# Performance work log

Hardware: AMD Instinct MI355X
Metric: run time of the kernel (lower is better)

## Reference

```python
import jax, jax.numpy as jnp
import numpy as np

# near_sym_b (13,19)-tap biorthogonal level-1 DTCWT filters (Kingsbury)
H0O = np.array([-0.0017578125, 0.0, 0.022265625, -0.046875, -0.0482421875,
                0.296875, 0.5554687500, 0.296875, -0.0482421875, -0.046875,
                0.022265625, 0.0, -0.0017578125], dtype=np.float32)
H1O = np.array([-7.0626e-05, 0.0, 1.34189e-03, -1.88341e-03, -7.15660e-03,
                2.38560e-02, 5.56431e-02, -5.16881e-02, -2.99758e-01,
                5.59431e-01, -2.99758e-01, -5.16881e-02, 5.56431e-02,
                2.38560e-02, -7.15660e-03, -1.88341e-03, 1.34189e-03,
                0.0, -7.0626e-05], dtype=np.float32)

def _alt(h):
    c = (len(h) - 1) // 2
    return (h * ((-1.0) ** (np.arange(len(h)) - c))).astype(np.float32)

G0O = _alt(H1O)  # synthesis lowpass  (PR complement of H1O)
G1O = _alt(H0O)  # synthesis highpass (PR complement of H0O)

DIM, HS, WS, BATCH, NB, BS = 64, 56, 56, 32, 4, 16


def _filt(x, h, axis):
    # depthwise 1D correlation with symmetric padding; x: (B,C,H,W), axis in {2,3}
    L = len(h); p = L // 2
    pad = [(0, 0)] * 4; pad[axis] = (p, p)
    xp = jnp.pad(x, pad, mode='symmetric')
    k = jnp.asarray(h, x.dtype).reshape((1, 1, L, 1) if axis == 2 else (1, 1, 1, L))
    B, C = x.shape[:2]
    y = jax.lax.conv_general_dilated(
        xp.reshape((B * C, 1) + xp.shape[2:]), k, (1, 1), 'VALID',
        dimension_numbers=('NCHW', 'OIHW', 'NCHW'))
    return y.reshape((B, C) + y.shape[2:])


def _q2c(y):
    y = y * np.float32(1.0 / np.sqrt(2.0))
    a = y[..., 0::2, 0::2]; b = y[..., 0::2, 1::2]
    c = y[..., 1::2, 0::2]; d = y[..., 1::2, 1::2]
    return (a - d, b + c), (a + d, b - c)


def _c2q(w1r, w1i, w2r, w2i):
    sc = np.float32(1.0 / np.sqrt(2.0))
    B, C, Hh, Wh = w1r.shape
    top = jnp.stack([(w1r + w2r) * sc, (w1i + w2i) * sc], axis=-1).reshape(B, C, Hh, 2 * Wh)
    bot = jnp.stack([(w1i - w2i) * sc, (w2r - w1r) * sc], axis=-1).reshape(B, C, Hh, 2 * Wh)
    return jnp.stack([top, bot], axis=3).reshape(B, C, 2 * Hh, 2 * Wh)


def dtcwt_fwd_j1(x):
    lo = _filt(x, H0O, 3); hi = _filt(x, H1O, 3)
    ll = _filt(lo, H0O, 2)
    (d15r, d15i), (d165r, d165i) = _q2c(_filt(lo, H1O, 2))   # LH -> 15/165 deg
    (d75r, d75i), (d105r, d105i) = _q2c(_filt(hi, H0O, 2))   # HL -> 75/105 deg
    (d45r, d45i), (d135r, d135i) = _q2c(_filt(hi, H1O, 2))   # HH -> 45/135 deg
    real = jnp.stack([d15r, d45r, d75r, d105r, d135r, d165r], axis=2)
    imag = jnp.stack([d15i, d45i, d75i, d105i, d135i, d165i], axis=2)
    return ll, jnp.stack([real, imag], axis=-1)  # (B,C,H,W), (B,C,6,H/2,W/2,2)


def dtcwt_inv_j1(ll, yh):
    r = yh[..., 0]; im = yh[..., 1]
    lh = _c2q(r[:, :, 0], im[:, :, 0], r[:, :, 5], im[:, :, 5])
    hl = _c2q(r[:, :, 2], im[:, :, 2], r[:, :, 3], im[:, :, 3])
    hh = _c2q(r[:, :, 1], im[:, :, 1], r[:, :, 4], im[:, :, 4])
    lo = _filt(ll, G0O, 2) + _filt(lh, G1O, 2)
    hi = _filt(hl, G0O, 2) + _filt(hh, G1O, 2)
    return _filt(lo, G0O, 3) + _filt(hi, G1O, 3)


def setup_inputs():
    key = jax.random.key(0)
    ks = jax.random.split(key, 6)
    return {
        'x': jax.random.normal(ks[0], (BATCH, HS * WS, DIM), jnp.float32),
        'w_ll': jax.random.normal(ks[1], (DIM, HS, WS), jnp.float32) * 0.02,
        'w1': jax.random.normal(ks[2], (2, NB, BS, BS), jnp.float32) * 0.02,
        'w2': jax.random.normal(ks[3], (2, NB, BS, BS), jnp.float32) * 0.02,
        'b1': jax.random.normal(ks[4], (2, NB, BS), jnp.float32) * 0.02,
        'b2': jax.random.normal(ks[5], (2, NB, BS), jnp.float32) * 0.02,
        'H': HS, 'W': WS,
    }


def reference(x, w_ll, w1, w2, b1, b2, H, W):
    Bt, N, C = x.shape
    xi = jnp.transpose(x.reshape(Bt, H, W, C), (0, 3, 1, 2)).astype(jnp.float32)
    xl, xh = dtcwt_fwd_j1(xi)
    xl = xl * w_ll                                  # (B,C,H,W) * (C,H,W)
    Hh, Wh = H // 2, W // 2
    # (B,C,6,Hh,Wh,2) -> (2,B,6,Hh,Wh,C) -> split C into (NB,BS) blocks
    xh = jnp.transpose(xh, (5, 0, 2, 3, 4, 1)).reshape(2, Bt, 6, Hh, Wh, NB, BS)
    xr, xim = xh[0], xh[1]
    mul = lambda t, w: jnp.einsum('...bd,bdk->...bk', t, w)
    r1 = jax.nn.relu(mul(xr, w1[0]) - mul(xim, w1[1]) + b1[0])
    i1 = jax.nn.relu(mul(xr, w1[1]) + mul(xim, w1[0]) + b1[1])
    r2 = mul(r1, w2[0]) - mul(i1, w2[1]) + b2[0]
    i2 = mul(r1, w2[1]) + mul(i1, w2[0]) + b2[1]
    xh2 = jnp.stack([r2, i2], axis=-1).reshape(Bt, 6, Hh, Wh, C, 2)
    xh2 = jnp.transpose(xh2, (0, 4, 1, 2, 3, 5))    # (B,C,6,Hh,Wh,2)
    y = dtcwt_inv_j1(xl, xh2)
    return jnp.transpose(y, (0, 2, 3, 1)).reshape(Bt, N, C)
```

## Files before the change

### kernel.cpp

```cpp
#include <hip/hip_runtime.h>

#define BT 32
#define CH 64
#define HS 56
#define WS 56
#define HH 28
#define WH 28

namespace {
constexpr float ISQ2 = 0.70710678118654752440f;
constexpr float F_H0[13] = {-0.0017578125f, 0.0f, 0.022265625f, -0.046875f,
    -0.0482421875f, 0.296875f, 0.55546875f, 0.296875f, -0.0482421875f,
    -0.046875f, 0.022265625f, 0.0f, -0.0017578125f};
constexpr float F_H1[19] = {-7.0626e-05f, 0.0f, 0.00134189f, -0.00188341f,
    -0.0071566f, 0.023856f, 0.0556431f, -0.0516881f, -0.299758f, 0.559431f,
    -0.299758f, -0.0516881f, 0.0556431f, 0.023856f, -0.0071566f,
    -0.00188341f, 0.00134189f, 0.0f, -7.0626e-05f};
constexpr float F_G0[19] = {7.0626e-05f, 0.0f, -0.00134189f, -0.00188341f,
    0.0071566f, 0.023856f, -0.0556431f, -0.0516881f, 0.299758f, 0.559431f,
    0.299758f, -0.0516881f, -0.0556431f, 0.023856f, 0.0071566f,
    -0.00188341f, -0.00134189f, 0.0f, 7.0626e-05f};
constexpr float F_G1[13] = {-0.0017578125f, 0.0f, 0.022265625f, 0.046875f,
    -0.0482421875f, -0.296875f, 0.55546875f, -0.296875f, -0.0482421875f,
    0.046875f, 0.022265625f, 0.0f, -0.0017578125f};
}

__device__ __forceinline__ int symi(int k) {
    k = (k < 0) ? (-1 - k) : k;
    k = (k >= HS) ? (2 * HS - 1 - k) : k;
    return k;
}

__device__ __forceinline__ unsigned short f2bf(float f) {
    unsigned u = __float_as_uint(f);
    u += 0x7fffu + ((u >> 16) & 1u);
    return (unsigned short)(u >> 16);
}
__device__ __forceinline__ float bf2f(unsigned short h) {
    return __uint_as_float(((unsigned)h) << 16);
}
__device__ __forceinline__ float2 bfp2(unsigned u) {
    float2 r;
    r.x = __uint_as_float((u & 0xffffu) << 16);
    r.y = __uint_as_float(u & 0xffff0000u);
    return r;
}
__device__ __forceinline__ unsigned packbf(float a, float b) {
    return (unsigned)f2bf(a) | ((unsigned)f2bf(b) << 16);
}

typedef __attribute__((ext_vector_type(8))) short short8;
typedef __attribute__((ext_vector_type(4))) float f32x4;

#define PPOS 784

__global__ __launch_bounds__(256) void k_fwd_rows(const float* __restrict__ x,
                                                  unsigned short* __restrict__ lo,
                                                  unsigned short* __restrict__ hi,
                                                  const float* __restrict__ wll,
                                                  float* __restrict__ wllT) {
    int b = blockIdx.x / HS, h = blockIdx.x % HS;
    int strip = threadIdx.x >> 5;
    int c0 = (threadIdx.x & 31) * 2;
    int base = (b * HS + h) * WS * CH + c0;
    const float* row = x + base;
    unsigned short* lop = lo + base;
    unsigned short* hip = hi + base;
    int w0s = strip * 7;
    float Wa[19], Wb[19];
#pragma unroll
    for (int t = 0; t < 19; ++t) {
        float2 v = *(const float2*)(row + symi(w0s - 9 + t) * CH);
        Wa[t] = v.x; Wb[t] = v.y;
    }
    float2 nW[7];
#pragma unroll
    for (int u = 0; u < 7; ++u) nW[u] = *(const float2*)(row + symi(w0s + u + 10) * CH);
#pragma unroll
    for (int u = 0; u < 7; ++u) {
        int w = w0s + u;
        float aLo = 0.f, aHi = 0.f, bLo = 0.f, bHi = 0.f;
#pragma unroll
        for (int t = 0; t < 13; ++t) { aLo += F_H0[t] * Wa[3 + t]; bLo += F_H0[t] * Wb[3 + t]; }
#pragma unroll
        for (int t = 0; t < 19; ++t) { aHi += F_H1[t] * Wa[t]; bHi += F_H1[t] * Wb[t]; }
        *(unsigned*)(lop + w * CH) = packbf(aLo, bLo);
        *(unsigned*)(hip + w * CH) = packbf(aHi, bHi);
#pragma unroll
        for (int t = 0; t < 18; ++t) { Wa[t] = Wa[t + 1]; Wb[t] = Wb[t + 1]; }
        Wa[18] = nW[u].x; Wb[18] = nW[u].y;
    }
    if (blockIdx.x < 49) {
        __shared__ float tile[64][65];
        int pos0 = blockIdx.x * 64;
        int lp = threadIdx.x & 63, g = threadIdx.x >> 6;
#pragma unroll
        for (int r = 0; r < 16; ++r) {
            int cc = r * 4 + g;
            tile[cc][lp] = wll[cc * (HS * WS) + pos0 + lp];
        }
        __syncthreads();
#pragma unroll
        for (int r = 0; r < 16; ++r) {
            int pl = r * 4 + g;
            wllT[(pos0 + pl) * CH + lp] = tile[lp][pl];
        }
    }
}

__global__ __launch_bounds__(256) void k_cols(
    const unsigned short* __restrict__ lo_in,
    const unsigned short* __restrict__ hi_in, const float* __restrict__ wllT,
    unsigned short* __restrict__ xl, unsigned short* __restrict__ sbT) {
    __shared__ unsigned short qTb[2][4][14][64];
    int hf = blockIdx.y;
    int zmode = blockIdx.z;
    int b = blockIdx.x / WH, wp = blockIdx.x % WH;
    int w0 = 2 * wp, tid = threadIdx.x;
    int q = tid >> 6, c = tid & 63;
    int rp = q >> 1, jc = q & 1;
    const unsigned short* srcp = zmode ? hi_in : lo_in;
    const unsigned short* colbase = srcp + (b * HS) * WS * CH + (w0 + jc) * CH + c;
    {
        int hstart = 2 * (hf * 14) + rp;
        float W[19];
#pragma unroll
        for (int t = 0; t < 19; ++t) W[t] = bf2f(colbase[symi(hstart - 9 + t) * (WS * CH)]);
        for (int rnd = 0; rnd < 2; ++rnd) {
            float nW0[7], nW1[7], nwll[7];
            int ii0 = rnd * 7;
#pragma unroll
            for (int u = 0; u < 7; ++u) {
                int h = hstart + 2 * (ii0 + u);
                nW0[u] = bf2f(colbase[symi(h + 10) * (WS * CH)]);
                nW1[u] = bf2f(colbase[symi(h + 11) * (WS * CH)]);
            }
            if (zmode == 0) {
#pragma unroll
                for (int u = 0; u < 7; ++u)
                    nwll[u] = wllT[((hstart + 2 * (ii0 + u)) * WS + (w0 + jc)) * CH + c];
            }
#pragma unroll
            for (int u = 0; u < 7; ++u) {
                int ii = ii0 + u;
                int h = hstart + 2 * ii;
                float v0 = 0.f, v1 = 0.f;
#pragma unroll
                for (int t = 0; t < 13; ++t) v0 += F_H0[t] * W[3 + t];
#pragma unroll
                for (int t = 0; t < 19; ++t) v1 += F_H1[t] * W[t];
                if (zmode == 0) {
                    xl[((b * HS + h) * WS + (w0 + jc)) * CH + c] = f2bf(v0 * nwll[u]);
                    qTb[0][q][ii][c] = f2bf(v1);
                } else {
                    qTb[0][q][ii][c] = f2bf(v0);
                    qTb[1][q][ii][c] = f2bf(v1);
                }
#pragma unroll
                for (int t = 0; t < 17; ++t) W[t] = W[t + 2];
                W[17] = nW0[u];
                W[18] = nW1[u];
            }
        }
    }
    __syncthreads();
    {
        int qq = tid >> 5;
        int role = qq & 3, half = qq >> 2;
        int c0 = (tid & 31) * 2;
        int rowA = role & 1, rowB = 3 - (role & 1);
        float sgn = (role == 1 || role == 2) ? 1.f : -1.f;
        int posb = wp * 28 + hf * 14;
        if (zmode == 0) {
            int p = (role < 2) ? role : role + 8;
            unsigned short* dst = sbT + ((p * BT + b) * PPOS + posb) * CH + c0;
#pragma unroll
            for (int g = 0; g < 7; ++g) {
                int ii = half * 7 + g;
                float2 av = bfp2(*(const unsigned*)&qTb[0][rowA][ii][c0]);
                float2 bv = bfp2(*(const unsigned*)&qTb[0][rowB][ii][c0]);
                float v0 = (av.x + sgn * bv.x) * ISQ2;
                float v1 = (av.y + sgn * bv.y) * ISQ2;
                *(unsigned*)(dst + ii * CH) = packbf(v0, v1);
            }
        } else {
#pragma unroll
            for (int src = 0; src < 2; ++src) {
                int p = (src == 0) ? (4 + role) : ((role < 2) ? (2 + role) : (6 + role));
                unsigned short* dst = sbT + ((p * BT + b) * PPOS + posb) * CH + c0;
#pragma unroll
                for (int g = 0; g < 7; ++g) {
                    int ii = half * 7 + g;
                    float2 av = bfp2(*(const unsigned*)&qTb[src][rowA][ii][c0]);
                    float2 bv = bfp2(*(const unsigned*)&qTb[src][rowB][ii][c0]);
                    float v0 = (av.x + sgn * bv.x) * ISQ2;
                    float v1 = (av.y + sgn * bv.y) * ISQ2;
                    *(unsigned*)(dst + ii * CH) = packbf(v0, v1);
                }
            }
        }
    }
}

__global__ __launch_bounds__(256) void k_mix(
    const unsigned short* __restrict__ sbT, const float* __restrict__ w1,
    const float* __restrict__ w2, const float* __restrict__ b1,
    const float* __restrict__ b2, unsigned short* __restrict__ P0,
    unsigned short* __restrict__ P1, unsigned short* __restrict__ P2) {
    __shared__ unsigned short l1a[4][16][36];
    __shared__ unsigned short l1b[4][16][36];
    int blk = blockIdx.x;
    int pr = blk / (BT * 49);
    int rem = blk % (BT * 49);
    int b = rem / 49;
    int tile = rem % 49;
    int sa = (pr == 0) ? 0 : (pr == 1) ? 2 : 1;
    int sb = (pr == 0) ? 5 : (pr == 1) ? 3 : 4;
    unsigned short* Pd = (pr == 0) ? P0 : (pr == 1) ? P1 : P2;
    int tid = threadIdx.x;
    int lane = tid & 63;
    int wv = tid >> 6;
    int nb = __builtin_amdgcn_readfirstlane(wv);
    int quad = lane >> 4;
    int n = lane & 15;

    int rix = quad >> 1, dlo = (quad & 1) * 8;
    int pos0 = tile * 16;
    const unsigned short* pAa =
        sbT + (((sa * 2 + rix) * BT + b) * PPOS + pos0 + n) * CH + nb * 16 + dlo;
    const unsigned short* pAb =
        sbT + (((sb * 2 + rix) * BT + b) * PPOS + pos0 + n) * CH + nb * 16 + dlo;
    short8 A1a = *(const short8*)pAa;
    short8 A1b = *(const short8*)pAb;

    short8 B1r, B1i, B2r, B2i;
#pragma unroll
    for (int j = 0; j < 8; ++j) {
        int kk = quad * 8 + j;
        int riw = kk >> 4, dd = kk & 15;
        float v1r = w1[nb * 256 + dd * 16 + n];
        float v1i = w1[1024 + nb * 256 + dd * 16 + n];
        float v2r = w2[nb * 256 + dd * 16 + n];
        float v2i = w2[1024 + nb * 256 + dd * 16 + n];
        B1r[j] = (short)f2bf(riw ? -v1i : v1r);
        B1i[j] = (short)f2bf(riw ? v1r : v1i);
        B2r[j] = (short)f2bf(riw ? -v2i : v2r);
        B2i[j] = (short)f2bf(riw ? v2r : v2i);
    }
    float bias1r = b1[nb * 16 + n], bias1i = b1[64 + nb * 16 + n];
    float bias2r = b2[nb * 16 + n], bias2i = b2[64 + nb * 16 + n];

    f32x4 a1r = {bias1r, bias1r, bias1r, bias1r};
    f32x4 a1i = {bias1i, bias1i, bias1i, bias1i};
    f32x4 b1r_ = a1r, b1i_ = a1i;
    a1r = __builtin_amdgcn_mfma_f32_16x16x32_bf16(A1a, B1r, a1r, 0, 0, 0);
    a1i = __builtin_amdgcn_mfma_f32_16x16x32_bf16(A1a, B1i, a1i, 0, 0, 0);
    b1r_ = __builtin_amdgcn_mfma_f32_16x16x32_bf16(A1b, B1r, b1r_, 0, 0, 0);
    b1i_ = __builtin_amdgcn_mfma_f32_16x16x32_bf16(A1b, B1i, b1i_, 0, 0, 0);
#pragma unroll
    for (int r = 0; r < 4; ++r) {
        int pos = quad * 4 + r;
        l1a[wv][pos][n] = f2bf(fmaxf(a1r[r], 0.f));
        l1a[wv][pos][16 + n] = f2bf(fmaxf(a1i[r], 0.f));
        l1b[wv][pos][n] = f2bf(fmaxf(b1r_[r], 0.f));
        l1b[wv][pos][16 + n] = f2bf(fmaxf(b1i_[r], 0.f));
    }
    union { short8 s8; uint2 u2[2]; } a2a, a2b;
    const unsigned short* rowpa = &l1a[wv][n][0];
    const unsigned short* rowpb = &l1b[wv][n][0];
    a2a.u2[0] = *(const uint2*)(rowpa + quad * 8);
    a2a.u2[1] = *(const uint2*)(rowpa + quad * 8 + 4);
    a2b.u2[0] = *(const uint2*)(rowpb + quad * 8);
    a2b.u2[1] = *(const uint2*)(rowpb + quad * 8 + 4);
    f32x4 aAr = {bias2r, bias2r, bias2r, bias2r};
    f32x4 aAi = {bias2i, bias2i, bias2i, bias2i};
    f32x4 aBr = aAr, aBi = aAi;
    aAr = __builtin_amdgcn_mfma_f32_16x16x32_bf16(a2a.s8, B2r, aAr, 0, 0, 0);
    aAi = __builtin_amdgcn_mfma_f32_16x16x32_bf16(a2a.s8, B2i, aAi, 0, 0, 0);
    aBr = __builtin_amdgcn_mfma_f32_16x16x32_bf16(a2b.s8, B2r, aBr, 0, 0, 0);
    aBi = __builtin_amdgcn_mfma_f32_16x16x32_bf16(a2b.s8, B2i, aBi, 0, 0, 0);
#pragma unroll
    for (int r = 0; r < 4; ++r) {
        int pos_g = pos0 + quad * 4 + r;
        int wp = pos_g / 28, ii = pos_g - wp * 28;
        int o = ((b * HS + 2 * ii) * WS + 2 * wp) * CH + nb * 16 + n;
        Pd[o] = f2bf((aAr[r] + aBr[r]) * ISQ2);
        Pd[o + CH] = f2bf((aAi[r] + aBi[r]) * ISQ2);
        Pd[o + WS * CH] = f2bf((aAi[r] - aBi[r]) * ISQ2);
        Pd[o + WS * CH + CH] = f2bf((aBr[r] - aAr[r]) * ISQ2);
    }
}

template <int MODE>
__device__ __forceinline__ void inv_cols_body(
    const unsigned short* __restrict__ xl, const unsigned short* __restrict__ P0,
    const unsigned short* __restrict__ P1, const unsigned short* __restrict__ P2,
    unsigned short* __restrict__ lo2, unsigned short* __restrict__ hi2) {
    int hf = blockIdx.y;
    int b = blockIdx.x / 7, wg = blockIdx.x % 7;
    int wl = threadIdx.x >> 5, l = threadIdx.x & 31;
    int c0 = l * 2;
    int w = wg * 8 + wl;
    int base = (b * HS) * WS * CH + w * CH + c0;
    const int st = WS * CH;
    const unsigned short* Ap = (MODE == 0) ? xl : P1;
    const unsigned short* Bp = (MODE == 0) ? P0 : P2;
    unsigned short* outp = (MODE == 0) ? lo2 : hi2;
    auto ldA = [&](int r) -> float2 {
        return bfp2(*(const unsigned*)(Ap + base + r * st));
    };
    auto ldB = [&](int r) -> float2 {
        return bfp2(*(const unsigned*)(Bp + base + r * st));
    };
    int h0 = hf * 14;
    float Aa[19], Ab[19], Ba[13], Bb[13];
#pragma unroll
    for (int t = 0; t < 19; ++t) { float2 v = ldA(symi(h0 - 9 + t)); Aa[t] = v.x; Ab[t] = v.y; }
#pragma unroll
    for (int t = 0; t < 13; ++t) { float2 v = ldB(symi(h0 - 6 + t)); Ba[t] = v.x; Bb[t] = v.y; }
    float2 pa0[4], pb0[4], pa1[4], pb1[4];
#define LDG(bA, bB, OFF, CNT)                                                   \
    {                                                                           \
        _Pragma("unroll") for (int u = 0; u < (CNT); ++u)                       \
            bA[u] = ldA(symi(h0 + (OFF) + u + 10));                             \
        _Pragma("unroll") for (int u = 0; u < (CNT); ++u)                       \
            bB[u] = ldB(symi(h0 + (OFF) + u + 7));                              \
    }
#define CPG(bA, bB, OFF, CNT)                                                   \
    {                                                                           \
        _Pragma("unroll") for (int u = 0; u < (CNT); ++u) {                     \
            int h = h0 + (OFF) + u;                                             \
            float acca = 0.f, accb = 0.f;                                       \
            _Pragma("unroll") for (int t = 0; t < 19; ++t) {                    \
                acca += F_G0[t] * Aa[t]; accb += F_G0[t] * Ab[t];               \
            }                                                                   \
            _Pragma("unroll") for (int t = 0; t < 13; ++t) {                    \
                acca += F_G1[t] * Ba[t]; accb += F_G1[t] * Bb[t];               \
            }                                                                   \
            *(unsigned*)(outp + base + h * st) = packbf(acca, accb);            \
            _Pragma("unroll") for (int t = 0; t < 18; ++t) {                    \
                Aa[t] = Aa[t + 1]; Ab[t] = Ab[t + 1];                           \
            }                                                                   \
            _Pragma("unroll") for (int t = 0; t < 12; ++t) {                    \
                Ba[t] = Ba[t + 1]; Bb[t] = Bb[t + 1];                           \
            }                                                                   \
            Aa[18] = bA[u].x; Ab[18] = bA[u].y;                                 \
            Ba[12] = bB[u].x; Bb[12] = bB[u].y;                                 \
        }                                                                       \
    }
    LDG(pa0, pb0, 0, 4) LDG(pa1, pb1, 4, 4)
    CPG(pa0, pb0, 0, 4) LDG(pa0, pb0, 8, 4)
    CPG(pa1, pb1, 4, 4) LDG(pa1, pb1, 12, 2)
    CPG(pa0, pb0, 8, 4)
    CPG(pa1, pb1, 12, 2)
#undef LDG
#undef CPG
}

__global__ __launch_bounds__(256) void k_inv_cols(
    const unsigned short* __restrict__ xl, const unsigned short* __restrict__ P0,
    const unsigned short* __restrict__ P1, const unsigned short* __restrict__ P2,
    unsigned short* __restrict__ lo2, unsigned short* __restrict__ hi2) {
    if (blockIdx.z == 0)
        inv_cols_body<0>(xl, P0, P1, P2, lo2, hi2);
    else
        inv_cols_body<1>(xl, P0, P1, P2, lo2, hi2);
}

__global__ __launch_bounds__(256) void k_inv_rows(
    const unsigned short* __restrict__ lo2,
    const unsigned short* __restrict__ hi2, float* __restrict__ out) {
    int b = blockIdx.x / HS, h = blockIdx.x % HS;
    int strip = threadIdx.x >> 5;
    int c0 = (threadIdx.x & 31) * 2;
    int base = (b * HS + h) * WS * CH + c0;
    const unsigned short* rlo = lo2 + base;
    const unsigned short* rhi = hi2 + base;
    float* op = out + base;
    int w0s = strip * 7;
    float Aa[19], Ab[19], Ba[13], Bb[13];
#pragma unroll
    for (int t = 0; t < 19; ++t) {
        float2 v = bfp2(*(const unsigned*)(rlo + symi(w0s - 9 + t) * CH));
        Aa[t] = v.x; Ab[t] = v.y;
    }
#pragma unroll
    for (int t = 0; t < 13; ++t) {
        float2 v = bfp2(*(const unsigned*)(rhi + symi(w0s - 6 + t) * CH));
        Ba[t] = v.x; Bb[t] = v.y;
    }
    float2 nA[7], nB[7];
#pragma unroll
    for (int u = 0; u < 7; ++u) nA[u] = bfp2(*(const unsigned*)(rlo + symi(w0s + u + 10) * CH));
#pragma unroll
    for (int u = 0; u < 7; ++u) nB[u] = bfp2(*(const unsigned*)(rhi + symi(w0s + u + 7) * CH));
#pragma unroll
    for (int u = 0; u < 7; ++u) {
        int w = w0s + u;
        float acca = 0.f, accb = 0.f;
#pragma unroll
        for (int t = 0; t < 19; ++t) { acca += F_G0[t] * Aa[t]; accb += F_G0[t] * Ab[t]; }
#pragma unroll
        for (int t = 0; t < 13; ++t) { acca += F_G1[t] * Ba[t]; accb += F_G1[t] * Bb[t]; }
        float2 ov; ov.x = acca; ov.y = accb;
        *(float2*)(op + w * CH) = ov;
#pragma unroll
        for (int t = 0; t < 18; ++t) { Aa[t] = Aa[t + 1]; Ab[t] = Ab[t + 1]; }
#pragma unroll
        for (int t = 0; t < 12; ++t) { Ba[t] = Ba[t + 1]; Bb[t] = Bb[t + 1]; }
        Aa[18] = nA[u].x; Ab[18] = nA[u].y;
        Ba[12] = nB[u].x; Bb[12] = nB[u].y;
    }
}

extern "C" void kernel_launch(void* const* d_in, const int* in_sizes, int n_in,
                              void* d_out, int out_size, void* d_ws, size_t ws_size,
                              hipStream_t stream) {
    const float* x = (const float*)d_in[0];
    const float* w_ll = (const float*)d_in[1];
    const float* w1 = (const float*)d_in[2];
    const float* w2 = (const float*)d_in[3];
    const float* b1 = (const float*)d_in[4];
    const float* b2 = (const float*)d_in[5];
    float* out = (float*)d_out;

    const size_t A = (size_t)BT * HS * WS * CH;
    const size_t SBf = (size_t)12 * 64 * BT * PPOS / 2;
    float* wsf = (float*)d_ws;
    unsigned short* xl = (unsigned short*)wsf;
    unsigned short* sbT = (unsigned short*)(wsf + A);
    unsigned short* lo2 = (unsigned short*)(wsf + A);
    unsigned short* hi2 = (unsigned short*)(wsf + A + SBf);
    unsigned short* lo_in = (unsigned short*)(wsf + A + SBf + A);
    unsigned short* hi_in = lo_in + A;
    unsigned short* P0 = hi_in + A;
    unsigned short* P1 = P0 + A;
    unsigned short* P2 = P1 + A;

    float* wllT = out;

    k_fwd_rows<<<BT * HS, 256, 0, stream>>>(x, lo_in, hi_in, w_ll, wllT);
    k_cols<<<dim3(BT * WH, 2, 2), 256, 0, stream>>>(lo_in, hi_in, wllT, xl, sbT);
    k_mix<<<3 * BT * 49, 256, 0, stream>>>(sbT, w1, w2, b1, b2, P0, P1, P2);
    k_inv_cols<<<dim3(BT * 7, 4, 2), 256, 0, stream>>>(xl, P0, P1, P2, lo2, hi2);
    k_inv_rows<<<BT * HS, 256, 0, stream>>>(lo2, hi2, out);
}
```

Baseline: 169.2 us.

## Fuse column filtering and complex channel-mix MLP into one kernel

Merges k_cols and k_mix so the subband quadrature outputs stay in LDS (pA) and feed the MFMA-based complex mixing directly, instead of being written to the sbT global buffer and read back. This removes one kernel launch and a full round trip of subband data through global memory. In exchange, each block handles only 14 positions per 16-row MFMA tile, so some MFMA work is wasted on padding rows. The l1a/l1b staging now aliases the qTb buffer after a barrier, and the mix work is split unevenly between the zmode blocks.

```diff
diff --git a/kernel.cpp b/kernel.cpp
--- a/kernel.cpp
+++ b/kernel.cpp
@@ -108,11 +108,19 @@
     }
 }
 
-__global__ __launch_bounds__(256) void k_cols(
+__global__ __launch_bounds__(256) void k_cols_mix(
     const unsigned short* __restrict__ lo_in,
     const unsigned short* __restrict__ hi_in, const float* __restrict__ wllT,
-    unsigned short* __restrict__ xl, unsigned short* __restrict__ sbT) {
-    __shared__ unsigned short qTb[2][4][14][64];
+    const float* __restrict__ w1, const float* __restrict__ w2,
+    const float* __restrict__ b1, const float* __restrict__ b2,
+    unsigned short* __restrict__ xl, unsigned short* __restrict__ P0,
+    unsigned short* __restrict__ P1, unsigned short* __restrict__ P2) {
+    __shared__ __align__(16) unsigned short qTb[2][4][14][64];
+    __shared__ __align__(16) unsigned short pA[8][14][72];
+    unsigned short (*l1a)[16][36] =
+        reinterpret_cast<unsigned short(*)[16][36]>(&qTb[0][0][0][0]);
+    unsigned short (*l1b)[16][36] = l1a + 4;
+
     int hf = blockIdx.y;
     int zmode = blockIdx.z;
     int b = blockIdx.x / WH, wp = blockIdx.x % WH;
@@ -170,10 +178,7 @@
         int c0 = (tid & 31) * 2;
         int rowA = role & 1, rowB = 3 - (role & 1);
         float sgn = (role == 1 || role == 2) ? 1.f : -1.f;
-        int posb = wp * 28 + hf * 14;
         if (zmode == 0) {
-            int p = (role < 2) ? role : role + 8;
-            unsigned short* dst = sbT + ((p * BT + b) * PPOS + posb) * CH + c0;
 #pragma unroll
             for (int g = 0; g < 7; ++g) {
                 int ii = half * 7 + g;
@@ -181,13 +186,12 @@
                 float2 bv = bfp2(*(const unsigned*)&qTb[0][rowB][ii][c0]);
                 float v0 = (av.x + sgn * bv.x) * ISQ2;
                 float v1 = (av.y + sgn * bv.y) * ISQ2;
-                *(unsigned*)(dst + ii * CH) = packbf(v0, v1);
+                *(unsigned*)&pA[role][ii][c0] = packbf(v0, v1);
             }
         } else {
 #pragma unroll
             for (int src = 0; src < 2; ++src) {
-                int p = (src == 0) ? (4 + role) : ((role < 2) ? (2 + role) : (6 + role));
-                unsigned short* dst = sbT + ((p * BT + b) * PPOS + posb) * CH + c0;
+                int pl = (src == 0) ? (2 + role) : ((role < 2) ? role : (4 + role));
 #pragma unroll
                 for (int g = 0; g < 7; ++g) {
                     int ii = half * 7 + g;
@@ -195,43 +199,21 @@
                     float2 bv = bfp2(*(const unsigned*)&qTb[src][rowB][ii][c0]);
                     float v0 = (av.x + sgn * bv.x) * ISQ2;
                     float v1 = (av.y + sgn * bv.y) * ISQ2;
-                    *(unsigned*)(dst + ii * CH) = packbf(v0, v1);
+                    *(unsigned*)&pA[pl][ii][c0] = packbf(v0, v1);
                 }
             }
         }
     }
-}
-
-__global__ __launch_bounds__(256) void k_mix(
-    const unsigned short* __restrict__ sbT, const float* __restrict__ w1,
-    const float* __restrict__ w2, const float* __restrict__ b1,
-    const float* __restrict__ b2, unsigned short* __restrict__ P0,
-    unsigned short* __restrict__ P1, unsigned short* __restrict__ P2) {
-    __shared__ unsigned short l1a[4][16][36];
-    __shared__ unsigned short l1b[4][16][36];
-    int blk = blockIdx.x;
-    int pr = blk / (BT * 49);
-    int rem = blk % (BT * 49);
-    int b = rem / 49;
-    int tile = rem % 49;
-    int sa = (pr == 0) ? 0 : (pr == 1) ? 2 : 1;
-    int sb = (pr == 0) ? 5 : (pr == 1) ? 3 : 4;
-    unsigned short* Pd = (pr == 0) ? P0 : (pr == 1) ? P1 : P2;
-    int tid = threadIdx.x;
+    __syncthreads();
+
     int lane = tid & 63;
     int wv = tid >> 6;
     int nb = __builtin_amdgcn_readfirstlane(wv);
     int quad = lane >> 4;
     int n = lane & 15;
-
     int rix = quad >> 1, dlo = (quad & 1) * 8;
-    int pos0 = tile * 16;
-    const unsigned short* pAa =
-        sbT + (((sa * 2 + rix) * BT + b) * PPOS + pos0 + n) * CH + nb * 16 + dlo;
-    const unsigned short* pAb =
-        sbT + (((sb * 2 + rix) * BT + b) * PPOS + pos0 + n) * CH + nb * 16 + dlo;
-    short8 A1a = *(const short8*)pAa;
-    short8 A1b = *(const short8*)pAb;
+    int chb = nb * 16 + dlo;
+    int npos = (n < 14) ? n : 0;
 
     short8 B1r, B1i, B2r, B2i;
 #pragma unroll
@@ -250,44 +232,57 @@
     float bias1r = b1[nb * 16 + n], bias1i = b1[64 + nb * 16 + n];
     float bias2r = b2[nb * 16 + n], bias2i = b2[64 + nb * 16 + n];
 
-    f32x4 a1r = {bias1r, bias1r, bias1r, bias1r};
-    f32x4 a1i = {bias1i, bias1i, bias1i, bias1i};
-    f32x4 b1r_ = a1r, b1i_ = a1i;
-    a1r = __builtin_amdgcn_mfma_f32_16x16x32_bf16(A1a, B1r, a1r, 0, 0, 0);
-    a1i = __builtin_amdgcn_mfma_f32_16x16x32_bf16(A1a, B1i, a1i, 0, 0, 0);
-    b1r_ = __builtin_amdgcn_mfma_f32_16x16x32_bf16(A1b, B1r, b1r_, 0, 0, 0);
-    b1i_ = __builtin_amdgcn_mfma_f32_16x16x32_bf16(A1b, B1i, b1i_, 0, 0, 0);
-#pragma unroll
-    for (int r = 0; r < 4; ++r) {
-        int pos = quad * 4 + r;
-        l1a[wv][pos][n] = f2bf(fmaxf(a1r[r], 0.f));
-        l1a[wv][pos][16 + n] = f2bf(fmaxf(a1i[r], 0.f));
-        l1b[wv][pos][n] = f2bf(fmaxf(b1r_[r], 0.f));
-        l1b[wv][pos][16 + n] = f2bf(fmaxf(b1i_[r], 0.f));
-    }
-    union { short8 s8; uint2 u2[2]; } a2a, a2b;
-    const unsigned short* rowpa = &l1a[wv][n][0];
-    const unsigned short* rowpb = &l1b[wv][n][0];
-    a2a.u2[0] = *(const uint2*)(rowpa + quad * 8);
-    a2a.u2[1] = *(const uint2*)(rowpa + quad * 8 + 4);
-    a2b.u2[0] = *(const uint2*)(rowpb + quad * 8);
-    a2b.u2[1] = *(const uint2*)(rowpb + quad * 8 + 4);
-    f32x4 aAr = {bias2r, bias2r, bias2r, bias2r};
-    f32x4 aAi = {bias2i, bias2i, bias2i, bias2i};
-    f32x4 aBr = aAr, aBi = aAi;
-    aAr = __builtin_amdgcn_mfma_f32_16x16x32_bf16(a2a.s8, B2r, aAr, 0, 0, 0);
-    aAi = __builtin_amdgcn_mfma_f32_16x16x32_bf16(a2a.s8, B2i, aAi, 0, 0, 0);
-    aBr = __builtin_amdgcn_mfma_f32_16x16x32_bf16(a2b.s8, B2r, aBr, 0, 0, 0);
-    aBi = __builtin_amdgcn_mfma_f32_16x16x32_bf16(a2b.s8, B2i, aBi, 0, 0, 0);
-#pragma unroll
-    for (int r = 0; r < 4; ++r) {
-        int pos_g = pos0 + quad * 4 + r;
-        int wp = pos_g / 28, ii = pos_g - wp * 28;
-        int o = ((b * HS + 2 * ii) * WS + 2 * wp) * CH + nb * 16 + n;
-        Pd[o] = f2bf((aAr[r] + aBr[r]) * ISQ2);
-        Pd[o + CH] = f2bf((aAi[r] + aBi[r]) * ISQ2);
-        Pd[o + WS * CH] = f2bf((aAi[r] - aBi[r]) * ISQ2);
-        Pd[o + WS * CH + CH] = f2bf((aBr[r] - aAr[r]) * ISQ2);
+    auto mixprod = [&](int aP, int bP, unsigned short* __restrict__ Pd) {
+        short8 A1a = *(const short8*)&pA[aP][npos][chb];
+        short8 A1b = *(const short8*)&pA[bP][npos][chb];
+        f32x4 a1r = {bias1r, bias1r, bias1r, bias1r};
+        f32x4 a1i = {bias1i, bias1i, bias1i, bias1i};
+        f32x4 b1r_ = a1r, b1i_ = a1i;
+        a1r = __builtin_amdgcn_mfma_f32_16x16x32_bf16(A1a, B1r, a1r, 0, 0, 0);
+        a1i = __builtin_amdgcn_mfma_f32_16x16x32_bf16(A1a, B1i, a1i, 0, 0, 0);
+        b1r_ = __builtin_amdgcn_mfma_f32_16x16x32_bf16(A1b, B1r, b1r_, 0, 0, 0);
+        b1i_ = __builtin_amdgcn_mfma_f32_16x16x32_bf16(A1b, B1i, b1i_, 0, 0, 0);
+#pragma unroll
+        for (int r = 0; r < 4; ++r) {
+            int pos = quad * 4 + r;
+            l1a[wv][pos][n] = f2bf(fmaxf(a1r[r], 0.f));
+            l1a[wv][pos][16 + n] = f2bf(fmaxf(a1i[r], 0.f));
+            l1b[wv][pos][n] = f2bf(fmaxf(b1r_[r], 0.f));
+            l1b[wv][pos][16 + n] = f2bf(fmaxf(b1i_[r], 0.f));
+        }
+        union { short8 s8; uint2 u2[2]; } a2a, a2b;
+        const unsigned short* rowpa = &l1a[wv][n][0];
+        const unsigned short* rowpb = &l1b[wv][n][0];
+        a2a.u2[0] = *(const uint2*)(rowpa + quad * 8);
+        a2a.u2[1] = *(const uint2*)(rowpa + quad * 8 + 4);
+        a2b.u2[0] = *(const uint2*)(rowpb + quad * 8);
+        a2b.u2[1] = *(const uint2*)(rowpb + quad * 8 + 4);
+        f32x4 aAr = {bias2r, bias2r, bias2r, bias2r};
+        f32x4 aAi = {bias2i, bias2i, bias2i, bias2i};
+        f32x4 aBr = aAr, aBi = aAi;
+        aAr = __builtin_amdgcn_mfma_f32_16x16x32_bf16(a2a.s8, B2r, aAr, 0, 0, 0);
+        aAi = __builtin_amdgcn_mfma_f32_16x16x32_bf16(a2a.s8, B2i, aAi, 0, 0, 0);
+        aBr = __builtin_amdgcn_mfma_f32_16x16x32_bf16(a2b.s8, B2r, aBr, 0, 0, 0);
+        aBi = __builtin_amdgcn_mfma_f32_16x16x32_bf16(a2b.s8, B2i, aBi, 0, 0, 0);
+#pragma unroll
+        for (int r = 0; r < 4; ++r) {
+            int m = quad * 4 + r;
+            if (m < 14) {
+                int iig = hf * 14 + m;
+                int o = ((b * HS + 2 * iig) * WS + 2 * wp) * CH + nb * 16 + n;
+                Pd[o] = f2bf((aAr[r] + aBr[r]) * ISQ2);
+                Pd[o + CH] = f2bf((aAi[r] + aBi[r]) * ISQ2);
+                Pd[o + WS * CH] = f2bf((aAi[r] - aBi[r]) * ISQ2);
+                Pd[o + WS * CH + CH] = f2bf((aBr[r] - aAr[r]) * ISQ2);
+            }
+        }
+    };
+
+    if (zmode == 0) {
+        mixprod(rix, 2 + rix, P0);
+    } else {
+        mixprod(2 + rix, 4 + rix, P1);
+        mixprod(rix, 6 + rix, P2);
     }
 }
 
@@ -428,7 +423,6 @@
     const size_t SBf = (size_t)12 * 64 * BT * PPOS / 2;
     float* wsf = (float*)d_ws;
     unsigned short* xl = (unsigned short*)wsf;
-    unsigned short* sbT = (unsigned short*)(wsf + A);
     unsigned short* lo2 = (unsigned short*)(wsf + A);
     unsigned short* hi2 = (unsigned short*)(wsf + A + SBf);
     unsigned short* lo_in = (unsigned short*)(wsf + A + SBf + A);
@@ -440,8 +434,8 @@
     float* wllT = out;
 
     k_fwd_rows<<<BT * HS, 256, 0, stream>>>(x, lo_in, hi_in, w_ll, wllT);
-    k_cols<<<dim3(BT * WH, 2, 2), 256, 0, stream>>>(lo_in, hi_in, wllT, xl, sbT);
-    k_mix<<<3 * BT * 49, 256, 0, stream>>>(sbT, w1, w2, b1, b2, P0, P1, P2);
+    k_cols_mix<<<dim3(BT * WH, 2, 2), 256, 0, stream>>>(lo_in, hi_in, wllT, w1,
+                                                        w2, b1, b2, xl, P0, P1, P2);
     k_inv_cols<<<dim3(BT * 7, 4, 2), 256, 0, stream>>>(xl, P0, P1, P2, lo2, hi2);
     k_inv_rows<<<BT * HS, 256, 0, stream>>>(lo2, hi2, out);
 }
```

New measurement: 162.8 us. 3.8% less time.
